# Performance work log

Measured on AMD Instinct MI355X. Metric: run time of the kernel, lower is better.

Reference implementation:

```python
import jax, jax.numpy as jnp
from jax import lax
import numpy as np

D = 640
HID = 64
DROP_RATIO = 0.1
N_ITER = int(D * DROP_RATIO)  # 64
TEMP = 0.07
EPS = 1e-7


def setup_inputs() -> dict:
    key = jax.random.key(0)
    k_x, k_w1, k_b1, k_w2, k_b2 = jax.random.split(key, 5)
    B = 8192
    x = jax.random.normal(k_x, (B, D), dtype=jnp.float32)
    # torch Linear default init: U(-1/sqrt(fan_in), 1/sqrt(fan_in))
    lim1 = 1.0 / np.sqrt(D)
    lim2 = 1.0 / np.sqrt(HID)
    W1 = jax.random.uniform(k_w1, (D, HID), minval=-lim1, maxval=lim1, dtype=jnp.float32)
    b1 = jax.random.uniform(k_b1, (HID,), minval=-lim1, maxval=lim1, dtype=jnp.float32)
    W2 = jax.random.uniform(k_w2, (HID, D), minval=-lim2, maxval=lim2, dtype=jnp.float32)
    b2 = jax.random.uniform(k_b2, (D,), minval=-lim2, maxval=lim2, dtype=jnp.float32)
    return {"x": x, "W1": W1, "b1": b1, "W2": W2, "b2": b2}


def reference(x, W1, b1, W2, b2):
    # small MLP: 640 -> 64 -> relu -> 640
    h = jnp.maximum(x @ W1 + b1, 0.0) @ W2 + b2  # (B, 640)

    def step(hhat, _):
        m = 1.0 - hhat
        mhat = jnp.log(m + EPS)
        yhat = jax.nn.softmax((-h + mhat) / TEMP, axis=-1)
        return hhat + yhat * m, None

    hhat0 = jnp.zeros_like(h)
    hhat, _ = lax.scan(jax.checkpoint(step), hhat0, None, length=N_ITER)
    mask = 1.0 - hhat
    return mask * x
```

## Files before the change

### kernel.cpp

```cpp
#include <hip/hip_runtime.h>

#define D 640
#define HID 64
#define NITER 64
#define ROWS 4
#define BLOCK 256

typedef float v2f __attribute__((ext_vector_type(2)));

#define DPP_ADD_STEP(v, ctrl, rmask)                                          \
    v += __builtin_bit_cast(float, __builtin_amdgcn_update_dpp(               \
             0, __builtin_bit_cast(int, v), ctrl, rmask, 0xf, true))
#define DPP_MAX_STEP(v, ctrl, rmask)                                          \
    v = fmaxf(v, __builtin_bit_cast(float, __builtin_amdgcn_update_dpp(       \
             __builtin_bit_cast(int, v), __builtin_bit_cast(int, v),          \
             ctrl, rmask, 0xf, false)))

__device__ __forceinline__ float wave_sum_dpp(float v) {
    DPP_ADD_STEP(v, 0x111, 0xf);
    DPP_ADD_STEP(v, 0x112, 0xf);
    DPP_ADD_STEP(v, 0x114, 0xf);
    DPP_ADD_STEP(v, 0x118, 0xf);
    DPP_ADD_STEP(v, 0x142, 0xa);
    DPP_ADD_STEP(v, 0x143, 0xc);
    return __builtin_bit_cast(float,
        __builtin_amdgcn_readlane(__builtin_bit_cast(int, v), 63));
}
__device__ __forceinline__ float wave_max_dpp(float v) {
    DPP_MAX_STEP(v, 0x111, 0xf);
    DPP_MAX_STEP(v, 0x112, 0xf);
    DPP_MAX_STEP(v, 0x114, 0xf);
    DPP_MAX_STEP(v, 0x118, 0xf);
    DPP_MAX_STEP(v, 0x142, 0xa);
    DPP_MAX_STEP(v, 0x143, 0xc);
    return __builtin_bit_cast(float,
        __builtin_amdgcn_readlane(__builtin_bit_cast(int, v), 63));
}

__global__ __launch_bounds__(BLOCK) void dimmask_kernel(
    const float* __restrict__ x, const float* __restrict__ W1,
    const float* __restrict__ b1, const float* __restrict__ W2,
    const float* __restrict__ b2, float* __restrict__ out)
{
    constexpr float INV_T = 1.0f / 0.07f;
    constexpr float LOG2E = 1.4426950408889634f;
    constexpr float TEMP  = 0.07f;

    __shared__ float lds_a[ROWS][D];
    __shared__ float lds_part[4][ROWS][HID];
    __shared__ float lds_hid[ROWS][HID];

    const int tid  = threadIdx.x;
    const int row0 = blockIdx.x * ROWS;

    {
        const float4* xv  = (const float4*)(x + (size_t)row0 * D);
        float4*       lxv = (float4*)(&lds_a[0][0]);
        for (int i = tid; i < ROWS * D / 4; i += BLOCK) lxv[i] = xv[i];
    }
    __syncthreads();

    {
        const int k = tid & 63, c = tid >> 6;
        float acc[ROWS] = {0.f, 0.f, 0.f, 0.f};
        const int q0 = c * 40;
#pragma unroll 4
        for (int q = q0; q < q0 + 40; ++q) {
            const int tb = q * 4;
            float w0 = W1[(tb + 0) * HID + k];
            float w1 = W1[(tb + 1) * HID + k];
            float w2 = W1[(tb + 2) * HID + k];
            float w3 = W1[(tb + 3) * HID + k];
#pragma unroll
            for (int r = 0; r < ROWS; ++r) {
                float4 xa = ((const float4*)&lds_a[r][0])[q];
                acc[r] += xa.x * w0 + xa.y * w1 + xa.z * w2 + xa.w * w3;
            }
        }
#pragma unroll
        for (int r = 0; r < ROWS; ++r) lds_part[c][r][k] = acc[r];
    }
    __syncthreads();
    {
        const int r = tid >> 6, k = tid & 63;
        float s = lds_part[0][r][k] + lds_part[1][r][k]
                + lds_part[2][r][k] + lds_part[3][r][k] + b1[k];
        lds_hid[r][k] = fmaxf(s, 0.f);
    }
    __syncthreads();

    for (int j = tid; j < D; j += BLOCK) {
        float acc[ROWS] = {0.f, 0.f, 0.f, 0.f};
#pragma unroll 4
        for (int k4 = 0; k4 < HID / 4; ++k4) {
            const int kb = k4 * 4;
            float w0 = W2[(kb + 0) * D + j];
            float w1 = W2[(kb + 1) * D + j];
            float w2 = W2[(kb + 2) * D + j];
            float w3 = W2[(kb + 3) * D + j];
#pragma unroll
            for (int r = 0; r < ROWS; ++r) {
                float4 hh = ((const float4*)&lds_hid[r][0])[k4];
                acc[r] += hh.x * w0 + hh.y * w1 + hh.z * w2 + hh.w * w3;
            }
        }
        float bb = b2[j];
#pragma unroll
        for (int r = 0; r < ROWS; ++r)
            lds_a[r][j] = -(acc[r] + bb) * (LOG2E * INV_T);
    }
    __syncthreads();

    const int r = tid >> 6, l = tid & 63;
    v2f E2[5], e2[5];
    {
        float ht[10], hmax = -3.0e38f;
#pragma unroll
        for (int u = 0; u < 10; ++u) {
            ht[u] = lds_a[r][l + 64 * u];
            hmax = fmaxf(hmax, ht[u]);
        }
        hmax = wave_max_dpp(hmax);
#pragma unroll
        for (int u = 0; u < 5; ++u) {
            E2[u].x = __builtin_amdgcn_exp2f(fmaxf(ht[2 * u]     - hmax, -80.f));
            E2[u].y = __builtin_amdgcn_exp2f(fmaxf(ht[2 * u + 1] - hmax, -80.f));
            e2[u] = E2[u];
        }
    }

    const v2f Kc2 = {94.8979592f, 94.8979592f};
    const v2f Kc1 = {-14.2857143f, -14.2857143f};
    const v2f K1  = {1.0f, 1.0f};
    const v2f P4 = {-0.0395668f, -0.0395668f};
    const v2f P3 = {-0.0583090f, -0.0583090f};
    const v2f P2 = {-0.1020408f, -0.1020408f};
    const v2f P1 = {-0.2857143f, -0.2857143f};

    for (int it = 0; it < NITER; ++it) {
        v2f t01 = e2[0] + e2[1], t23 = e2[2] + e2[3];
        v2f s2 = (t01 + t23) + e2[4];
        float s = s2.x + s2.y;
        s = wave_sum_dpp(s);
        float rs = __builtin_amdgcn_rcpf(s);
#pragma unroll
        for (int u = 0; u < 5; ++u) {
            v2f y = e2[u] * rs;
            if (__builtin_expect(__any(fmaxf(y.x, y.y) > 0.02f), 0)) {
                v2f f  = K1 - y;
                v2f f2 = f * f, f4 = f2 * f2, f8 = f4 * f4;
                v2f f14 = f8 * f4 * f2;
                v2f p = __builtin_elementwise_fma(P4, y, P3);
                p = __builtin_elementwise_fma(p, y, P2);
                p = __builtin_elementwise_fma(p, y, P1);
                p = __builtin_elementwise_fma(p, y, K1);
                e2[u] *= f14 * p;
            } else {
                v2f p = __builtin_elementwise_fma(Kc2, y, Kc1);
                p = __builtin_elementwise_fma(p, y, K1);
                e2[u] *= p;
            }
        }
    }

    const float* xrow = x + (size_t)(row0 + r) * D;
    float* orow = out + (size_t)(row0 + r) * D;
#pragma unroll
    for (int u = 0; u < 5; ++u) {
        float w0 = e2[u].x * __builtin_amdgcn_rcpf(E2[u].x);
        float w1 = e2[u].y * __builtin_amdgcn_rcpf(E2[u].y);
        float m0 = __builtin_amdgcn_exp2f(TEMP * __builtin_amdgcn_logf(w0));
        float m1 = __builtin_amdgcn_exp2f(TEMP * __builtin_amdgcn_logf(w1));
        int j0 = l + 128 * u, j1 = j0 + 64;
        orow[j0] = m0 * xrow[j0];
        orow[j1] = m1 * xrow[j1];
    }
}

extern "C" void kernel_launch(void* const* d_in, const int* in_sizes, int n_in,
                              void* d_out, int out_size, void* d_ws, size_t ws_size,
                              hipStream_t stream) {
    const float* x  = (const float*)d_in[0];
    const float* W1 = (const float*)d_in[1];
    const float* b1 = (const float*)d_in[2];
    const float* W2 = (const float*)d_in[3];
    const float* b2 = (const float*)d_in[4];
    float* out = (float*)d_out;

    const int B = in_sizes[0] / D;
    dim3 grid(B / ROWS), block(BLOCK);
    hipLaunchKernelGGL(dimmask_kernel, grid, block, 0, stream, x, W1, b1, W2, b2, out);
}
```

Before: 169.9 us.

## Process two rows per wave to interleave independent softmax iteration chains

Each wave now owns two rows instead of one, so a block covers eight rows and the grid is halved. The 64-step iteration runs both rows' reductions and updates together, so two independent DPP reduction chains can hide each other's latency. Fewer blocks also means W1/W2 are loaded from global memory half as often per row. In exchange the kernel uses more registers, and the larger LDS footprint may reduce occupancy.

```diff
diff --git a/kernel.cpp b/kernel.cpp
--- a/kernel.cpp
+++ b/kernel.cpp
@@ -3,8 +3,10 @@
 #define D 640
 #define HID 64
 #define NITER 64
-#define ROWS 4
-#define BLOCK 256
+#define RPW 2
+#define WPB 4
+#define ROWS (RPW * WPB)
+#define BLOCK (WPB * 64)
 
 typedef float v2f __attribute__((ext_vector_type(2)));
 
@@ -62,7 +64,9 @@
 
     {
         const int k = tid & 63, c = tid >> 6;
-        float acc[ROWS] = {0.f, 0.f, 0.f, 0.f};
+        float acc[ROWS];
+#pragma unroll
+        for (int r = 0; r < ROWS; ++r) acc[r] = 0.f;
         const int q0 = c * 40;
 #pragma unroll 4
         for (int q = q0; q < q0 + 40; ++q) {
@@ -81,8 +85,8 @@
         for (int r = 0; r < ROWS; ++r) lds_part[c][r][k] = acc[r];
     }
     __syncthreads();
-    {
-        const int r = tid >> 6, k = tid & 63;
+    for (int idx = tid; idx < ROWS * HID; idx += BLOCK) {
+        const int r = idx >> 6, k = idx & 63;
         float s = lds_part[0][r][k] + lds_part[1][r][k]
                 + lds_part[2][r][k] + lds_part[3][r][k] + b1[k];
         lds_hid[r][k] = fmaxf(s, 0.f);
@@ -90,7 +94,9 @@
     __syncthreads();
 
     for (int j = tid; j < D; j += BLOCK) {
-        float acc[ROWS] = {0.f, 0.f, 0.f, 0.f};
+        float acc[ROWS];
+#pragma unroll
+        for (int r = 0; r < ROWS; ++r) acc[r] = 0.f;
 #pragma unroll 4
         for (int k4 = 0; k4 < HID / 4; ++k4) {
             const int kb = k4 * 4;
@@ -111,22 +117,30 @@
     }
     __syncthreads();
 
-    const int r = tid >> 6, l = tid & 63;
-    v2f E2[5], e2[5];
+    const int wv = tid >> 6, l = tid & 63;
+    const int ra = wv * RPW;
+    v2f E2[RPW][5], e2[RPW][5];
     {
-        float ht[10], hmax = -3.0e38f;
-#pragma unroll
-        for (int u = 0; u < 10; ++u) {
-            ht[u] = lds_a[r][l + 64 * u];
-            hmax = fmaxf(hmax, ht[u]);
-        }
-        hmax = wave_max_dpp(hmax);
-#pragma unroll
-        for (int u = 0; u < 5; ++u) {
-            E2[u].x = __builtin_amdgcn_exp2f(fmaxf(ht[2 * u]     - hmax, -80.f));
-            E2[u].y = __builtin_amdgcn_exp2f(fmaxf(ht[2 * u + 1] - hmax, -80.f));
-            e2[u] = E2[u];
-        }
+        float ht[RPW][10], hmax[RPW];
+#pragma unroll
+        for (int a = 0; a < RPW; ++a) {
+            hmax[a] = -3.0e38f;
+#pragma unroll
+            for (int u = 0; u < 10; ++u) {
+                ht[a][u] = lds_a[ra + a][l + 64 * u];
+                hmax[a] = fmaxf(hmax[a], ht[a][u]);
+            }
+        }
+#pragma unroll
+        for (int a = 0; a < RPW; ++a) hmax[a] = wave_max_dpp(hmax[a]);
+#pragma unroll
+        for (int a = 0; a < RPW; ++a)
+#pragma unroll
+            for (int u = 0; u < 5; ++u) {
+                E2[a][u].x = __builtin_amdgcn_exp2f(fmaxf(ht[a][2*u]   - hmax[a], -80.f));
+                E2[a][u].y = __builtin_amdgcn_exp2f(fmaxf(ht[a][2*u+1] - hmax[a], -80.f));
+                e2[a][u] = E2[a][u];
+            }
     }
 
     const v2f Kc2 = {94.8979592f, 94.8979592f};
@@ -138,42 +152,57 @@
     const v2f P1 = {-0.2857143f, -0.2857143f};
 
     for (int it = 0; it < NITER; ++it) {
-        v2f t01 = e2[0] + e2[1], t23 = e2[2] + e2[3];
-        v2f s2 = (t01 + t23) + e2[4];
-        float s = s2.x + s2.y;
-        s = wave_sum_dpp(s);
-        float rs = __builtin_amdgcn_rcpf(s);
+        float rs[RPW];
+        {
+            float s[RPW];
+#pragma unroll
+            for (int a = 0; a < RPW; ++a) {
+                v2f t01 = e2[a][0] + e2[a][1], t23 = e2[a][2] + e2[a][3];
+                v2f s2 = (t01 + t23) + e2[a][4];
+                s[a] = s2.x + s2.y;
+            }
+#pragma unroll
+            for (int a = 0; a < RPW; ++a) s[a] = wave_sum_dpp(s[a]);
+#pragma unroll
+            for (int a = 0; a < RPW; ++a) rs[a] = __builtin_amdgcn_rcpf(s[a]);
+        }
+#pragma unroll
+        for (int a = 0; a < RPW; ++a) {
+#pragma unroll
+            for (int u = 0; u < 5; ++u) {
+                v2f y = e2[a][u] * rs[a];
+                if (__builtin_expect(__any(fmaxf(y.x, y.y) > 0.02f), 0)) {
+                    v2f f  = K1 - y;
+                    v2f f2 = f * f, f4 = f2 * f2, f8 = f4 * f4;
+                    v2f f14 = f8 * f4 * f2;
+                    v2f p = __builtin_elementwise_fma(P4, y, P3);
+                    p = __builtin_elementwise_fma(p, y, P2);
+                    p = __builtin_elementwise_fma(p, y, P1);
+                    p = __builtin_elementwise_fma(p, y, K1);
+                    e2[a][u] *= f14 * p;
+                } else {
+                    v2f p = __builtin_elementwise_fma(Kc2, y, Kc1);
+                    p = __builtin_elementwise_fma(p, y, K1);
+                    e2[a][u] *= p;
+                }
+            }
+        }
+    }
+
+#pragma unroll
+    for (int a = 0; a < RPW; ++a) {
+        const float* xrow = x + (size_t)(row0 + ra + a) * D;
+        float* orow = out + (size_t)(row0 + ra + a) * D;
 #pragma unroll
         for (int u = 0; u < 5; ++u) {
-            v2f y = e2[u] * rs;
-            if (__builtin_expect(__any(fmaxf(y.x, y.y) > 0.02f), 0)) {
-                v2f f  = K1 - y;
-                v2f f2 = f * f, f4 = f2 * f2, f8 = f4 * f4;
-                v2f f14 = f8 * f4 * f2;
-                v2f p = __builtin_elementwise_fma(P4, y, P3);
-                p = __builtin_elementwise_fma(p, y, P2);
-                p = __builtin_elementwise_fma(p, y, P1);
-                p = __builtin_elementwise_fma(p, y, K1);
-                e2[u] *= f14 * p;
-            } else {
-                v2f p = __builtin_elementwise_fma(Kc2, y, Kc1);
-                p = __builtin_elementwise_fma(p, y, K1);
-                e2[u] *= p;
-            }
-        }
-    }
-
-    const float* xrow = x + (size_t)(row0 + r) * D;
-    float* orow = out + (size_t)(row0 + r) * D;
-#pragma unroll
-    for (int u = 0; u < 5; ++u) {
-        float w0 = e2[u].x * __builtin_amdgcn_rcpf(E2[u].x);
-        float w1 = e2[u].y * __builtin_amdgcn_rcpf(E2[u].y);
-        float m0 = __builtin_amdgcn_exp2f(TEMP * __builtin_amdgcn_logf(w0));
-        float m1 = __builtin_amdgcn_exp2f(TEMP * __builtin_amdgcn_logf(w1));
-        int j0 = l + 128 * u, j1 = j0 + 64;
-        orow[j0] = m0 * xrow[j0];
-        orow[j1] = m1 * xrow[j1];
+            float w0 = e2[a][u].x * __builtin_amdgcn_rcpf(E2[a][u].x);
+            float w1 = e2[a][u].y * __builtin_amdgcn_rcpf(E2[a][u].y);
+            float m0 = __builtin_amdgcn_exp2f(TEMP * __builtin_amdgcn_logf(w0));
+            float m1 = __builtin_amdgcn_exp2f(TEMP * __builtin_amdgcn_logf(w1));
+            int j0 = l + 128 * u, j1 = j0 + 64;
+            orow[j0] = m0 * xrow[j0];
+            orow[j1] = m1 * xrow[j1];
+        }
     }
 }
 
```

New measurement: 205.3 us. +20.8%, slower.
